# Performance work log

Measured on AMD Instinct MI355X. Metric: run time of the kernel, lower is better.

Reference implementation:

```python
import jax, jax.numpy as jnp
import numpy as np

N_RECV = 8192
N_DON = 32768
NAN_BIG = 1.0e10  # torch.nan_to_num replacement used before topk


def setup_inputs() -> dict:
    key = jax.random.key(0)
    k1, k2, k3 = jax.random.split(key, 3)
    dist_pot_donors = jax.random.uniform(k1, (N_RECV, N_DON), dtype=jnp.float32)
    fit_X_col = jax.random.normal(k2, (N_DON,), dtype=jnp.float32)
    mask_fit_X_col = jax.random.randint(k3, (N_DON,), 0, 2, dtype=jnp.int32)
    return {
        "dist_pot_donors": dist_pot_donors,
        "n_neighbors": 16,
        "fit_X_col": fit_X_col,
        "mask_fit_X_col": mask_fit_X_col,
    }


def reference(dist_pot_donors, n_neighbors, fit_X_col, mask_fit_X_col):
    # --- SubTopKIndices: k smallest along dim 1 (NaN treated as 1e10) ---
    xn = jnp.nan_to_num(dist_pot_donors, nan=NAN_BIG)
    _, donors_idx = jax.lax.top_k(-xn, n_neighbors)  # [R, k], ascending distance
    # --- SubDonorsIdx: gather ORIGINAL distances at selected indices ---
    donors_dist = jnp.take_along_axis(dist_pot_donors, donors_idx, axis=1)  # [R, k]
    # --- SubWeightMatrix with weights='distance' ---
    w = 1.0 / donors_dist
    inf_mask = jnp.isinf(w)
    inf_row = jnp.any(inf_mask, axis=1, keepdims=True)  # rows containing an exact-0 distance
    w = jnp.where(inf_row, inf_mask.astype(w.dtype), w)
    weight_matrix = jnp.where(jnp.isnan(w), jnp.zeros_like(w), w)
    # --- gather donor values and validity mask ---
    donors = fit_X_col[donors_idx]                       # [R, k]
    donors_mask = 1 - mask_fit_X_col[donors_idx]         # [R, k] int, 1 where donor value present
    # --- MakeNewWeights + masked weighted mean ---
    new_weights = donors_mask.astype(donors.dtype) * weight_matrix
    weights_sum = new_weights.sum(axis=1, keepdims=True)
    div = jnp.where(weights_sum == 0, jnp.ones_like(weights_sum), weights_sum)
    res = (donors * new_weights).sum(axis=1, keepdims=True) / div
    return res.squeeze(1).astype(dist_pot_donors.dtype)  # [R]
```

## Files before the change

### kernel.cpp

```cpp
#include <hip/hip_runtime.h>

#define NDON 32768
#define CAP  1024
#define K    16

__device__ __forceinline__ bool is_inf_f(float x) {
    return ((__float_as_uint(x) & 0x7fffffffu) == 0x7f800000u);
}
__device__ __forceinline__ bool is_nan_f(float x) {
    return ((__float_as_uint(x) & 0x7fffffffu) > 0x7f800000u);
}

__global__ __launch_bounds__(256, 8) void calc_impute_kernel(
    const float* __restrict__ dist,
    const float* __restrict__ fitcol,
    const int*  __restrict__ maskcol,
    float* __restrict__ out)
{
    __shared__ int   cnt;
    __shared__ float cv[CAP];
    __shared__ int   ci[CAP];
    __shared__ float wredv[4];
    __shared__ int   wredi[4];
    __shared__ int   wredp[4];
    __shared__ int   sel_idx[K];

    const int tid = threadIdx.x;
    const float* row = dist + (size_t)blockIdx.x * NDON;
    const float4* rp = reinterpret_cast<const float4*>(row) + tid;

    float thr = 0.004f;
    int n = 0;
    for (int attempt = 0; attempt < 20; ++attempt) {
        const bool nanpass = (thr > 1.0e10f);
        if (tid == 0) cnt = 0;
        __syncthreads();
        for (int it = 0; it < 8; ++it) {
            float4 v[4];
            #pragma unroll
            for (int u = 0; u < 4; ++u) v[u] = rp[it * 1024 + u * 256];
            #pragma unroll
            for (int u = 0; u < 4; ++u) {
                const float4 q = v[u];
                bool p0 = q.x < thr, p1 = q.y < thr, p2 = q.z < thr, p3 = q.w < thr;
                if (nanpass) {
                    p0 |= is_nan_f(q.x); p1 |= is_nan_f(q.y);
                    p2 |= is_nan_f(q.z); p3 |= is_nan_f(q.w);
                }
                if (p0 | p1 | p2 | p3) {
                    const int base = it * 4096 + u * 1024 + tid * 4;
                    const float vals[4] = {q.x, q.y, q.z, q.w};
                    const bool  ps[4]   = {p0, p1, p2, p3};
                    #pragma unroll
                    for (int j = 0; j < 4; ++j) {
                        if (ps[j]) {
                            const float sv = is_nan_f(vals[j]) ? 1.0e10f : vals[j];
                            const int p = atomicAdd(&cnt, 1);
                            if (p < CAP) { cv[p] = sv; ci[p] = base + j; }
                        }
                    }
                }
            }
        }
        __syncthreads();
        n = cnt;
        if (n >= K && n <= CAP) break;
        thr = (n < K) ? thr * 8.0f : thr * 0.125f;
        __syncthreads();
    }
    if (n > CAP) n = CAP;

    for (int s = 0; s < K; ++s) {
        float bv = 3.0e38f;
        int   bi = 0x7FFFFFFF;
        int   bp = -1;
        for (int p = tid; p < n; p += 256) {
            const float v = cv[p];
            const int   i = ci[p];
            if (v < bv || (v == bv && i < bi)) { bv = v; bi = i; bp = p; }
        }
        #pragma unroll
        for (int o = 32; o >= 1; o >>= 1) {
            const float ov = __shfl_down(bv, o);
            const int   oi = __shfl_down(bi, o);
            const int   op = __shfl_down(bp, o);
            if (ov < bv || (ov == bv && oi < bi)) { bv = ov; bi = oi; bp = op; }
        }
        if ((tid & 63) == 0) {
            const int w = tid >> 6;
            wredv[w] = bv; wredi[w] = bi; wredp[w] = bp;
        }
        __syncthreads();
        if (tid == 0) {
            #pragma unroll
            for (int w = 1; w < 4; ++w) {
                if (wredv[w] < bv || (wredv[w] == bv && wredi[w] < bi)) {
                    bv = wredv[w]; bi = wredi[w]; bp = wredp[w];
                }
            }
            sel_idx[s] = bi;
            if (bp >= 0) cv[bp] = 3.0e38f;
        }
        __syncthreads();
    }

    if (tid == 0) {
        float dsel[K];
        #pragma unroll
        for (int s = 0; s < K; ++s) dsel[s] = row[sel_idx[s]];

        bool infrow = false;
        #pragma unroll
        for (int s = 0; s < K; ++s) {
            const float wt = 1.0f / dsel[s];
            if (is_inf_f(wt)) infrow = true;
        }

        float wsum = 0.0f, dsum = 0.0f;
        #pragma unroll
        for (int s = 0; s < K; ++s) {
            const float wt = 1.0f / dsel[s];
            float wm;
            if (infrow) wm = is_inf_f(wt) ? 1.0f : 0.0f;
            else        wm = is_nan_f(wt) ? 0.0f : wt;
            const int   idx = sel_idx[s];
            const float dm  = 1.0f - (float)maskcol[idx];
            const float nw  = dm * wm;
            wsum += nw;
            dsum += fitcol[idx] * nw;
        }
        const float div = (wsum == 0.0f) ? 1.0f : wsum;
        out[blockIdx.x] = dsum / div;
    }
}

extern "C" void kernel_launch(void* const* d_in, const int* in_sizes, int n_in,
                              void* d_out, int out_size, void* d_ws, size_t ws_size,
                              hipStream_t stream) {
    const float* dist    = (const float*)d_in[0];
    const float* fitcol  = (const float*)d_in[2];
    const int*   maskcol = (const int*)d_in[3];
    float* out = (float*)d_out;

    calc_impute_kernel<<<dim3(out_size), dim3(256), 0, stream>>>(dist, fitcol, maskcol, out);
}
```

Baseline: 239.3 us.

## Move top-k selection to a single wavefront with register candidates and parallel epilogue

After candidate collection, only the first wavefront continues. It holds the first 128 candidates in registers and runs 16 rounds of xor-shuffle argmin, which removes the per-round block barriers and the cross-wave shared-memory reduction. The final weighted mean is computed across 16 lanes with a ballot and shuffle reduction instead of serially on thread 0. The initial threshold is lowered to 0.002 so fewer candidates are collected, at some added risk of needing a retry pass when too few pass.

```diff
diff --git a/kernel.cpp b/kernel.cpp
--- a/kernel.cpp
+++ b/kernel.cpp
@@ -3,6 +3,8 @@
 #define NDON 32768
 #define CAP  1024
 #define K    16
+#define BIGV 3.0e38f
+#define IMAX 0x7FFFFFFF
 
 __device__ __forceinline__ bool is_inf_f(float x) {
     return ((__float_as_uint(x) & 0x7fffffffu) == 0x7f800000u);
@@ -20,16 +22,12 @@
     __shared__ int   cnt;
     __shared__ float cv[CAP];
     __shared__ int   ci[CAP];
-    __shared__ float wredv[4];
-    __shared__ int   wredi[4];
-    __shared__ int   wredp[4];
-    __shared__ int   sel_idx[K];
 
     const int tid = threadIdx.x;
     const float* row = dist + (size_t)blockIdx.x * NDON;
     const float4* rp = reinterpret_cast<const float4*>(row) + tid;
 
-    float thr = 0.004f;
+    float thr = 0.002f;
     int n = 0;
     for (int attempt = 0; attempt < 20; ++attempt) {
         const bool nanpass = (thr > 1.0e10f);
@@ -70,68 +68,60 @@
     }
     if (n > CAP) n = CAP;
 
+    if (tid >= 64) return;
+    const int lane = tid;
+
+    float rv0 = (lane < n)      ? cv[lane]      : BIGV;
+    int   ri0 = (lane < n)      ? ci[lane]      : IMAX;
+    float rv1 = (lane + 64 < n) ? cv[lane + 64] : BIGV;
+    int   ri1 = (lane + 64 < n) ? ci[lane + 64] : IMAX;
+    const bool big = (n > 128);
+
+    int my_sel = 0;
+    #pragma unroll
     for (int s = 0; s < K; ++s) {
-        float bv = 3.0e38f;
-        int   bi = 0x7FFFFFFF;
-        int   bp = -1;
-        for (int p = tid; p < n; p += 256) {
-            const float v = cv[p];
-            const int   i = ci[p];
-            if (v < bv || (v == bv && i < bi)) { bv = v; bi = i; bp = p; }
+        float bv; int bi; int bp = -1;
+        if (rv1 < rv0 || (rv1 == rv0 && ri1 < ri0)) { bv = rv1; bi = ri1; }
+        else                                        { bv = rv0; bi = ri0; }
+        if (big) {
+            for (int p = 128 + lane; p < n; p += 64) {
+                const float v = cv[p]; const int i = ci[p];
+                if (v < bv || (v == bv && i < bi)) { bv = v; bi = i; bp = p; }
+            }
         }
         #pragma unroll
-        for (int o = 32; o >= 1; o >>= 1) {
-            const float ov = __shfl_down(bv, o);
-            const int   oi = __shfl_down(bi, o);
-            const int   op = __shfl_down(bp, o);
+        for (int o = 1; o < 64; o <<= 1) {
+            const float ov = __shfl_xor(bv, o);
+            const int   oi = __shfl_xor(bi, o);
+            const int   op = __shfl_xor(bp, o);
             if (ov < bv || (ov == bv && oi < bi)) { bv = ov; bi = oi; bp = op; }
         }
-        if ((tid & 63) == 0) {
-            const int w = tid >> 6;
-            wredv[w] = bv; wredi[w] = bi; wredp[w] = bp;
-        }
-        __syncthreads();
-        if (tid == 0) {
-            #pragma unroll
-            for (int w = 1; w < 4; ++w) {
-                if (wredv[w] < bv || (wredv[w] == bv && wredi[w] < bi)) {
-                    bv = wredv[w]; bi = wredi[w]; bp = wredp[w];
-                }
-            }
-            sel_idx[s] = bi;
-            if (bp >= 0) cv[bp] = 3.0e38f;
-        }
-        __syncthreads();
+        if (ri0 == bi) { rv0 = BIGV; ri0 = IMAX; }
+        if (ri1 == bi) { rv1 = BIGV; ri1 = IMAX; }
+        if (big && bp >= 0 && lane == 0) { cv[bp] = BIGV; ci[bp] = IMAX; }
+        if (lane == s) my_sel = bi;
     }
 
-    if (tid == 0) {
-        float dsel[K];
-        #pragma unroll
-        for (int s = 0; s < K; ++s) dsel[s] = row[sel_idx[s]];
-
-        bool infrow = false;
-        #pragma unroll
-        for (int s = 0; s < K; ++s) {
-            const float wt = 1.0f / dsel[s];
-            if (is_inf_f(wt)) infrow = true;
-        }
-
-        float wsum = 0.0f, dsum = 0.0f;
-        #pragma unroll
-        for (int s = 0; s < K; ++s) {
-            const float wt = 1.0f / dsel[s];
-            float wm;
-            if (infrow) wm = is_inf_f(wt) ? 1.0f : 0.0f;
-            else        wm = is_nan_f(wt) ? 0.0f : wt;
-            const int   idx = sel_idx[s];
-            const float dm  = 1.0f - (float)maskcol[idx];
-            const float nw  = dm * wm;
-            wsum += nw;
-            dsum += fitcol[idx] * nw;
-        }
-        const float div = (wsum == 0.0f) ? 1.0f : wsum;
-        out[blockIdx.x] = dsum / div;
+    const bool act = (lane < K);
+    const int  idx = my_sel;
+    const float d  = act ? row[idx] : 1.0f;
+    const float wt = 1.0f / d;
+    const bool  winf = act && is_inf_f(wt);
+    const unsigned long long m = __ballot(winf);
+    const bool infrow = (m != 0ull);
+    float wm = infrow ? (winf ? 1.0f : 0.0f)
+                      : (is_nan_f(wt) ? 0.0f : wt);
+    if (!act) wm = 0.0f;
+    const float dm = act ? 1.0f - (float)maskcol[idx] : 0.0f;
+    const float fv = act ? fitcol[idx] : 0.0f;
+    const float nw = dm * wm;
+    float ws = nw, ds = fv * nw;
+    #pragma unroll
+    for (int o = 1; o < K; o <<= 1) {
+        ws += __shfl_xor(ws, o);
+        ds += __shfl_xor(ds, o);
     }
+    if (lane == 0) out[blockIdx.x] = ds / ((ws == 0.0f) ? 1.0f : ws);
 }
 
 extern "C" void kernel_launch(void* const* d_in, const int* in_sizes, int n_in,
```

New measurement: 195.3 us. 18.4% less time.
